# Kernel tuning notes

Measured on AMD Instinct MI355X. Metric: run time of the kernel, lower is better.

## Reference

```python
import jax, jax.numpy as jnp
import numpy as np

THRESHOLD = 0.5
NEG_POS_RATIO = 3
ALPHA = 1.0
B, P, C, O = 128, 8732, 21, 32


def xy_to_cxcy(xy):
    return jnp.concatenate([(xy[..., 2:] + xy[..., :2]) / 2, xy[..., 2:] - xy[..., :2]], axis=-1)


def cxcy_to_xy(cxcy):
    return jnp.concatenate([cxcy[..., :2] - cxcy[..., 2:] / 2, cxcy[..., :2] + cxcy[..., 2:] / 2], axis=-1)


def cxcy_to_gcxgcy(cxcy, priors_cxcy):
    g_cxcy = (cxcy[..., :2] - priors_cxcy[..., :2]) / (priors_cxcy[..., 2:] / 10.0)
    g_wh = jnp.log(cxcy[..., 2:] / priors_cxcy[..., 2:]) * 5.0
    return jnp.concatenate([g_cxcy, g_wh], axis=-1)


def find_jaccard_overlap(set1, set2):
    # set1: [O,4] xy, set2: [P,4] xy -> [O,P]
    lo = jnp.maximum(set1[:, None, :2], set2[None, :, :2])
    hi = jnp.minimum(set1[:, None, 2:], set2[None, :, 2:])
    inter = jnp.prod(jnp.clip(hi - lo, 0.0), axis=-1)
    a1 = jnp.prod(set1[:, 2:] - set1[:, :2], axis=-1)
    a2 = jnp.prod(set2[:, 2:] - set2[:, :2], axis=-1)
    union = a1[:, None] + a2[None, :] - inter
    return inter / union


def setup_inputs() -> dict:
    key = jax.random.key(0)
    k0, k1, k2, k3, k4, k5, k6 = jax.random.split(key, 7)
    predicted_locs = jax.random.normal(k0, (B, P, 4), jnp.float32)
    predicted_scores = jax.random.normal(k1, (B, P, C), jnp.float32)
    centers = jax.random.uniform(k2, (B, O, 2), jnp.float32, 0.2, 0.8)
    sizes = jax.random.uniform(k3, (B, O, 2), jnp.float32, 0.05, 0.3)
    boxes = jnp.concatenate([centers - sizes / 2, centers + sizes / 2], axis=-1)
    labels = jax.random.randint(k4, (B, O), 0, C)
    p_c = jax.random.uniform(k5, (P, 2), jnp.float32, 0.05, 0.95)
    p_wh = jax.random.uniform(k6, (P, 2), jnp.float32, 0.05, 0.5)
    priors_cxcy = jnp.concatenate([p_c, p_wh], axis=-1)
    return {"predicted_locs": predicted_locs, "predicted_scores": predicted_scores,
            "boxes": boxes, "labels": labels, "priors_cxcy": priors_cxcy}


def reference(predicted_locs, predicted_scores, boxes, labels, priors_cxcy):
    priors_xy = cxcy_to_xy(priors_cxcy)

    def match_one(boxes_i, labels_i):
        overlap = find_jaccard_overlap(boxes_i, priors_xy)           # [O,P]
        overlap_for_each_prior = jnp.max(overlap, axis=0)            # [P]
        object_for_each_prior = jnp.argmax(overlap, axis=0)          # [P]
        prior_for_each_object = jnp.argmax(overlap, axis=1)          # [O]
        object_for_each_prior = object_for_each_prior.at[prior_for_each_object].set(jnp.arange(O))
        overlap_for_each_prior = overlap_for_each_prior.at[prior_for_each_object].set(1.0)
        label_for_each_prior = labels_i[object_for_each_prior]
        label_for_each_prior = jnp.where(overlap_for_each_prior < THRESHOLD, 0, label_for_each_prior)
        true_locs_i = cxcy_to_gcxgcy(xy_to_cxcy(boxes_i[object_for_each_prior]), priors_cxcy)
        return label_for_each_prior, true_locs_i

    true_classes, true_locs = jax.vmap(match_one)(boxes, labels)     # [B,P], [B,P,4]

    positive = true_classes != 0                                     # [B,P]
    n_positives = jnp.sum(positive, axis=1)                          # [B]
    n_pos_total = jnp.sum(n_positives)

    # L1Loss (mean over selected positive elements, 4 per prior)
    abs_diff = jnp.abs(predicted_locs - true_locs)                   # [B,P,4]
    loc_loss = jnp.sum(abs_diff * positive[..., None]) / (n_pos_total.astype(jnp.float32) * 4.0)

    # per-element cross-entropy
    log_p = jax.nn.log_softmax(predicted_scores, axis=-1)            # [B,P,C]
    conf_loss_all = -jnp.take_along_axis(log_p, true_classes[..., None], axis=-1)[..., 0]  # [B,P]

    conf_loss_pos_sum = jnp.sum(jnp.where(positive, conf_loss_all, 0.0))
    conf_loss_neg = jnp.where(positive, 0.0, conf_loss_all)
    conf_loss_neg_sorted = -jnp.sort(-conf_loss_neg, axis=1)         # descending
    n_hard = NEG_POS_RATIO * n_positives                             # [B]
    hard_mask = jnp.arange(P)[None, :] < n_hard[:, None]             # [B,P]
    conf_loss_hard_neg_sum = jnp.sum(jnp.where(hard_mask, conf_loss_neg_sorted, 0.0))

    conf_loss = (conf_loss_hard_neg_sum + conf_loss_pos_sum) / n_pos_total.astype(jnp.float32)
    return conf_loss + ALPHA * loc_loss
```

## Files before the change

### kernel.cpp

```cpp
#include <hip/hip_runtime.h>
#include <hip/hip_bf16.h>

#define NB 128
#define NP 8732
#define NO 32
#define NC 21
#define NCHUNK 35


__device__ __forceinline__ float wave64_fmax_u(float m) {
    int v;
    v = __builtin_amdgcn_update_dpp(__float_as_int(m), __float_as_int(m), 0x111, 0xf, 0xf, false);
    m = fmaxf(m, __int_as_float(v));
    v = __builtin_amdgcn_update_dpp(__float_as_int(m), __float_as_int(m), 0x112, 0xf, 0xf, false);
    m = fmaxf(m, __int_as_float(v));
    v = __builtin_amdgcn_update_dpp(__float_as_int(m), __float_as_int(m), 0x114, 0xf, 0xf, false);
    m = fmaxf(m, __int_as_float(v));
    v = __builtin_amdgcn_update_dpp(__float_as_int(m), __float_as_int(m), 0x118, 0xf, 0xf, false);
    m = fmaxf(m, __int_as_float(v));
    v = __builtin_amdgcn_update_dpp(__float_as_int(m), __float_as_int(m), 0x142, 0xf, 0xf, false);
    m = fmaxf(m, __int_as_float(v));
    v = __builtin_amdgcn_update_dpp(__float_as_int(m), __float_as_int(m), 0x143, 0xf, 0xf, false);
    m = fmaxf(m, __int_as_float(v));
    return __int_as_float(__builtin_amdgcn_readlane(__float_as_int(m), 63));
}

__device__ __forceinline__ int wave64_imin_u(int m) {
    int v;
    v = __builtin_amdgcn_update_dpp(m, m, 0x111, 0xf, 0xf, false); m = v < m ? v : m;
    v = __builtin_amdgcn_update_dpp(m, m, 0x112, 0xf, 0xf, false); m = v < m ? v : m;
    v = __builtin_amdgcn_update_dpp(m, m, 0x114, 0xf, 0xf, false); m = v < m ? v : m;
    v = __builtin_amdgcn_update_dpp(m, m, 0x118, 0xf, 0xf, false); m = v < m ? v : m;
    v = __builtin_amdgcn_update_dpp(m, m, 0x142, 0xf, 0xf, false); m = v < m ? v : m;
    v = __builtin_amdgcn_update_dpp(m, m, 0x143, 0xf, 0xf, false); m = v < m ? v : m;
    return __builtin_amdgcn_readlane(m, 63);
}

__global__ __launch_bounds__(256) void k_code(const float* __restrict__ boxes,
                                              const float* __restrict__ priors,
                                              int* __restrict__ code) {
    int b = blockIdx.y;
    int tid = threadIdx.x;
    int base = blockIdx.x * 512 + tid;

    __shared__ float4 sbox[NO];
    if (tid < NO)
        sbox[tid] = ((const float4*)(boxes + (size_t)b * NO * 4))[tid];
    __syncthreads();

    float px1[2], py1[2], px2[2], py2[2], pa[2];
    float bestv[2];
    int   besto[2];
#pragma unroll
    for (int j = 0; j < 2; ++j) {
        int p = base + 256 * j;
        int pp = p < NP ? p : NP - 1;
        float4 pr = ((const float4*)priors)[pp];
        px1[j] = pr.x - pr.z * 0.5f; py1[j] = pr.y - pr.w * 0.5f;
        px2[j] = pr.x + pr.z * 0.5f; py2[j] = pr.y + pr.w * 0.5f;
        pa[j]  = (px2[j] - px1[j]) * (py2[j] - py1[j]);
        bestv[j] = -1.0f; besto[j] = 0;
    }

#pragma unroll
    for (int o = 0; o < NO; ++o) {
        float4 bx = sbox[o];
        float a1 = (bx.z - bx.x) * (bx.w - bx.y);
#pragma unroll
        for (int j = 0; j < 2; ++j) {
            float lx = fmaxf(bx.x, px1[j]), ly = fmaxf(bx.y, py1[j]);
            float hx = fminf(bx.z, px2[j]), hy = fminf(bx.w, py2[j]);
            float iw = fmaxf(hx - lx, 0.0f), ih = fmaxf(hy - ly, 0.0f);
            float inter = iw * ih;
            float iou = inter / (a1 + pa[j] - inter);
            if (iou > bestv[j]) { bestv[j] = iou; besto[j] = o; }
        }
    }
#pragma unroll
    for (int j = 0; j < 2; ++j) {
        int p = base + 256 * j;
        if (p < NP)
            code[(size_t)b * NP + p] = besto[j] | (bestv[j] >= 0.5f ? 256 : 0);
    }
}

__global__ __launch_bounds__(256) void k_obj(const float* __restrict__ boxes,
                                             const float* __restrict__ priors,
                                             int* __restrict__ pfor) {
    int b = blockIdx.y;
    int wid = threadIdx.x >> 6, lane = threadIdx.x & 63;
    int o = blockIdx.x * 4 + wid;

    float4 bx = ((const float4*)boxes)[b * NO + o];
    float a1 = (bx.z - bx.x) * (bx.w - bx.y);
    const float4* pr4 = (const float4*)priors;

    float bv = -1.0f; int bp = 0;
    for (int i = 0; i < 136; ++i) {
        int p = lane + (i << 6);
        float4 pr = pr4[p];
        float x1 = pr.x - pr.z * 0.5f, y1 = pr.y - pr.w * 0.5f;
        float x2 = pr.x + pr.z * 0.5f, y2 = pr.y + pr.w * 0.5f;
        float pa = (x2 - x1) * (y2 - y1);
        float lx = fmaxf(bx.x, x1), ly = fmaxf(bx.y, y1);
        float hx = fminf(bx.z, x2), hy = fminf(bx.w, y2);
        float inter = fmaxf(hx - lx, 0.0f) * fmaxf(hy - ly, 0.0f);
        float iou = inter / (a1 + pa - inter);
        if (iou > bv) { bv = iou; bp = p; }
    }
    {
        int p = lane + 8704;
        if (p < NP) {
            float4 pr = pr4[p];
            float x1 = pr.x - pr.z * 0.5f, y1 = pr.y - pr.w * 0.5f;
            float x2 = pr.x + pr.z * 0.5f, y2 = pr.y + pr.w * 0.5f;
            float pa = (x2 - x1) * (y2 - y1);
            float lx = fmaxf(bx.x, x1), ly = fmaxf(bx.y, y1);
            float hx = fminf(bx.z, x2), hy = fminf(bx.w, y2);
            float inter = fmaxf(hx - lx, 0.0f) * fmaxf(hy - ly, 0.0f);
            float iou = inter / (a1 + pa - inter);
            if (iou > bv) { bv = iou; bp = p; }
        }
    }
    float m = wave64_fmax_u(bv);
    int pc = (bv == m) ? bp : 0x7FFFFFFF;
    int mp = wave64_imin_u(pc);
    if (lane == 0) pfor[b * NO + o] = mp;
}

__global__ __launch_bounds__(256) void k_loss(const float* __restrict__ plocs,
                                              const float* __restrict__ scores,
                                              const float* __restrict__ boxes,
                                              const int* __restrict__ labels,
                                              const float* __restrict__ priors,
                                              const int* __restrict__ code,
                                              const int* __restrict__ pfor,
                                              float* __restrict__ confneg,
                                              int* __restrict__ pnp,
                                              double* __restrict__ pd0,
                                              double* __restrict__ pd1,
                                              int* __restrict__ donecnt) {
    __shared__ float srow[256 * NC];
    __shared__ int spfl[NO];
    int b = blockIdx.y;
    int p0 = blockIdx.x * 256;
    int cnt = NP - p0; if (cnt > 256) cnt = 256;
    int nf4 = cnt * NC / 4;
    const float4* src4 = (const float4*)(scores + ((size_t)b * NP + p0) * NC);
    for (int i = threadIdx.x; i < nf4; i += 256)
        ((float4*)srow)[i] = src4[i];
    if (threadIdx.x < NO)
        spfl[threadIdx.x] = pfor[b * NO + threadIdx.x];
    __syncthreads();

    int p = p0 + threadIdx.x;
    float posconf = 0.0f, locpart = 0.0f;
    int isp = 0;

    if (p < NP) {
        int cd = code[(size_t)b * NP + p];
        int obj = cd & 255;
        int mat = cd >> 8;
#pragma unroll
        for (int o = 0; o < NO; ++o)
            if (spfl[o] == p) { obj = o; mat = 1; }
        int lbl = mat ? labels[b * NO + obj] : 0;

        const float* s = srow + threadIdx.x * NC;
        float m = s[0];
#pragma unroll
        for (int c = 1; c < NC; ++c) m = fmaxf(m, s[c]);
        float sum = 0.0f;
#pragma unroll
        for (int c = 0; c < NC; ++c) sum += __expf(s[c] - m);
        float conf = m + __logf(sum) - s[lbl];

        if (lbl != 0) {
            isp = 1;
            posconf = conf;
            float4 bx = ((const float4*)boxes)[b * NO + obj];
            float4 pr = ((const float4*)priors)[p];
            float cx = (bx.x + bx.z) * 0.5f, cy = (bx.y + bx.w) * 0.5f;
            float w = bx.z - bx.x, h = bx.w - bx.y;
            float gx = (cx - pr.x) / (pr.z * 0.1f);
            float gy = (cy - pr.y) / (pr.w * 0.1f);
            float gw = __logf(w / pr.z) * 5.0f;
            float gh = __logf(h / pr.w) * 5.0f;
            float4 pl = ((const float4*)plocs)[(size_t)b * NP + p];
            locpart = fabsf(pl.x - gx) + fabsf(pl.y - gy) +
                      fabsf(pl.z - gw) + fabsf(pl.w - gh);
        }
        confneg[(size_t)b * NP + p] = isp ? 0.0f : conf;
    }

    for (int s = 32; s > 0; s >>= 1) {
        posconf += __shfl_xor(posconf, s, 64);
        locpart += __shfl_xor(locpart, s, 64);
        isp     += __shfl_xor(isp, s, 64);
    }
    __shared__ float w0[4], w1[4];
    __shared__ int wc[4];
    int wid = threadIdx.x >> 6, lane = threadIdx.x & 63;
    if (lane == 0) { w0[wid] = posconf; w1[wid] = locpart; wc[wid] = isp; }
    __syncthreads();
    if (threadIdx.x == 0) {
        int pb = b * NCHUNK + blockIdx.x;
        pd0[pb] = (double)(w0[0] + w0[1] + w0[2] + w0[3]);
        pd1[pb] = (double)(w1[0] + w1[1] + w1[2] + w1[3]);
        pnp[pb] = wc[0] + wc[1] + wc[2] + wc[3];
        if (pb == 0) *donecnt = 0;
    }
}

__global__ __launch_bounds__(256) void k_topk(const float* __restrict__ confneg,
                                              const int* __restrict__ pnp,
                                              const double* __restrict__ pd0,
                                              const double* __restrict__ pd1,
                                              int* __restrict__ snp,
                                              double* __restrict__ sums,
                                              int* __restrict__ donecnt,
                                              float* __restrict__ out) {
    __shared__ int    si2[2][4];
    __shared__ int    siw[4];
    __shared__ double sdd[4];
    __shared__ int    sk;
    int tid = threadIdx.x, b = blockIdx.x;
    int lane = tid & 63, wid = tid >> 6;

    if (wid == 0) {
        int np_ = 0; double d0 = 0.0, d1 = 0.0;
        if (lane < NCHUNK) {
            int pb = b * NCHUNK + lane;
            np_ = pnp[pb]; d0 = pd0[pb]; d1 = pd1[pb];
        }
        for (int s = 32; s > 0; s >>= 1) {
            np_ += __shfl_xor(np_, s, 64);
            d0  += __shfl_xor(d0, s, 64);
            d1  += __shfl_xor(d1, s, 64);
        }
        if (lane == 0) {
            int k = np_ * 3; if (k > NP) k = NP;
            sk = k;
            snp[b] = np_;
            sums[b * 3 + 1] = d0;
            sums[b * 3 + 2] = d1;
        }
    }

    const float* src = confneg + (size_t)b * NP;
    float val[35];
#pragma unroll
    for (int j = 0; j < 35; ++j) {
        int i = tid + j * 256;
        val[j] = (i < NP) ? src[i] : 0.0f;
    }
    __syncthreads();
    int k = sk;

    double hn = 0.0;
    if (k > 0) {
        unsigned T = 0;
        int par = 0;
        for (int bit = 30; bit >= 0; --bit) {
            unsigned cand = T | (1u << bit);
            int cnt = 0;
#pragma unroll
            for (int j = 0; j < 35; ++j)
                cnt += __popcll(__ballot(__float_as_uint(val[j]) >= cand));
            if (lane == 0) si2[par][wid] = cnt;
            __syncthreads();
            int t = si2[par][0] + si2[par][1] + si2[par][2] + si2[par][3];
            par ^= 1;
            if (t >= k) T = cand;
        }

        int cgt = 0;
        double sgt = 0.0;
#pragma unroll
        for (int j = 0; j < 35; ++j) {
            unsigned u = __float_as_uint(val[j]);
            if (u > T) { cgt++; sgt += (double)val[j]; }
        }
        for (int s = 32; s > 0; s >>= 1) {
            cgt += __shfl_xor(cgt, s, 64);
            sgt += __shfl_xor(sgt, s, 64);
        }
        if (lane == 0) { siw[wid] = cgt; sdd[wid] = sgt; }
        __syncthreads();
        if (tid == 0) {
            int cg = siw[0] + siw[1] + siw[2] + siw[3];
            double sg = sdd[0] + sdd[1] + sdd[2] + sdd[3];
            hn = sg + (double)(k - cg) * (double)__uint_as_float(T);
        }
    }
    if (tid == 0) sums[b * 3 + 0] = hn;

    __shared__ int samlast;
    if (tid == 0) {
        __threadfence();
        int prev = atomicAdd(donecnt, 1);
        samlast = (prev == NB - 1) ? 1 : 0;
    }
    __syncthreads();
    if (!samlast) return;
    __threadfence();

    double hnn = 0.0, pc = 0.0, lc = 0.0, npd = 0.0;
    if (tid < NB) {
        hnn = atomicAdd(&sums[tid * 3 + 0], 0.0);
        pc  = atomicAdd(&sums[tid * 3 + 1], 0.0);
        lc  = atomicAdd(&sums[tid * 3 + 2], 0.0);
        npd = (double)atomicAdd((int*)&snp[tid], 0);
    }
    for (int s = 32; s > 0; s >>= 1) {
        hnn += __shfl_xor(hnn, s, 64);
        pc  += __shfl_xor(pc, s, 64);
        lc  += __shfl_xor(lc, s, 64);
        npd += __shfl_xor(npd, s, 64);
    }
    __shared__ double sfin[4][2];
    if (lane == 0 && wid < 2) {
        sfin[0][wid] = hnn; sfin[1][wid] = pc; sfin[2][wid] = lc; sfin[3][wid] = npd;
    }
    __syncthreads();
    if (tid == 0) {
        double H  = sfin[0][0] + sfin[0][1];
        double P  = sfin[1][0] + sfin[1][1];
        double L  = sfin[2][0] + sfin[2][1];
        double nt = sfin[3][0] + sfin[3][1];
        out[0] = (float)((H + P) / nt + L / (nt * 4.0));
    }
}

extern "C" void kernel_launch(void* const* d_in, const int* in_sizes, int n_in,
                              void* d_out, int out_size, void* d_ws, size_t ws_size,
                              hipStream_t stream) {
    const float* plocs  = (const float*)d_in[0];
    const float* scores = (const float*)d_in[1];
    const float* boxes  = (const float*)d_in[2];
    const int*   labels = (const int*)d_in[3];
    const float* priors = (const float*)d_in[4];
    float* out = (float*)d_out;

    char* ws = (char*)d_ws;
    int*    pfor    = (int*)ws;
    double* pd0     = (double*)(ws + 16384);
    double* pd1     = (double*)(ws + 52224);
    int*    pnp     = (int*)(ws + 88064);
    int*    snp     = (int*)(ws + 105984);
    double* sums    = (double*)(ws + 106496);
    int*    donecnt = (int*)(ws + 109568);
    int*    code    = (int*)(ws + 109824);
    float*  confneg = (float*)(ws + 4580608);

    hipLaunchKernelGGL(k_code, dim3((NP + 511) / 512, NB), dim3(256), 0, stream,
                       boxes, priors, code);
    hipLaunchKernelGGL(k_obj, dim3(NO / 4, NB), dim3(256), 0, stream,
                       boxes, priors, pfor);
    hipLaunchKernelGGL(k_loss, dim3(NCHUNK, NB), dim3(256), 0, stream,
                       plocs, scores, boxes, labels, priors, code, pfor,
                       confneg, pnp, pd0, pd1, donecnt);
    hipLaunchKernelGGL(k_topk, dim3(NB), dim3(256), 0, stream,
                       confneg, pnp, pd0, pd1, snp, sums, donecnt, out);
}
```

Before: 240.1 us.

## Fuse prior matching into loss kernel, tile k_obj over LDS, widen topk blocks

```diff
diff --git a/kernel.cpp b/kernel.cpp
--- a/kernel.cpp
+++ b/kernel.cpp
@@ -36,96 +36,59 @@
     return __builtin_amdgcn_readlane(m, 63);
 }
 
-__global__ __launch_bounds__(256) void k_code(const float* __restrict__ boxes,
-                                              const float* __restrict__ priors,
-                                              int* __restrict__ code) {
-    int b = blockIdx.y;
-    int tid = threadIdx.x;
-    int base = blockIdx.x * 512 + tid;
-
-    __shared__ float4 sbox[NO];
-    if (tid < NO)
-        sbox[tid] = ((const float4*)(boxes + (size_t)b * NO * 4))[tid];
-    __syncthreads();
-
-    float px1[2], py1[2], px2[2], py2[2], pa[2];
-    float bestv[2];
-    int   besto[2];
-#pragma unroll
-    for (int j = 0; j < 2; ++j) {
-        int p = base + 256 * j;
-        int pp = p < NP ? p : NP - 1;
-        float4 pr = ((const float4*)priors)[pp];
-        px1[j] = pr.x - pr.z * 0.5f; py1[j] = pr.y - pr.w * 0.5f;
-        px2[j] = pr.x + pr.z * 0.5f; py2[j] = pr.y + pr.w * 0.5f;
-        pa[j]  = (px2[j] - px1[j]) * (py2[j] - py1[j]);
-        bestv[j] = -1.0f; besto[j] = 0;
-    }
-
-#pragma unroll
-    for (int o = 0; o < NO; ++o) {
-        float4 bx = sbox[o];
-        float a1 = (bx.z - bx.x) * (bx.w - bx.y);
-#pragma unroll
-        for (int j = 0; j < 2; ++j) {
-            float lx = fmaxf(bx.x, px1[j]), ly = fmaxf(bx.y, py1[j]);
-            float hx = fminf(bx.z, px2[j]), hy = fminf(bx.w, py2[j]);
-            float iw = fmaxf(hx - lx, 0.0f), ih = fmaxf(hy - ly, 0.0f);
-            float inter = iw * ih;
-            float iou = inter / (a1 + pa[j] - inter);
-            if (iou > bestv[j]) { bestv[j] = iou; besto[j] = o; }
-        }
-    }
-#pragma unroll
-    for (int j = 0; j < 2; ++j) {
-        int p = base + 256 * j;
-        if (p < NP)
-            code[(size_t)b * NP + p] = besto[j] | (bestv[j] >= 0.5f ? 256 : 0);
-    }
-}
-
 __global__ __launch_bounds__(256) void k_obj(const float* __restrict__ boxes,
                                              const float* __restrict__ priors,
                                              int* __restrict__ pfor) {
+    __shared__ float4 spr[1024];
     int b = blockIdx.y;
-    int wid = threadIdx.x >> 6, lane = threadIdx.x & 63;
-    int o = blockIdx.x * 4 + wid;
-
-    float4 bx = ((const float4*)boxes)[b * NO + o];
-    float a1 = (bx.z - bx.x) * (bx.w - bx.y);
-    const float4* pr4 = (const float4*)priors;
-
-    float bv = -1.0f; int bp = 0;
-    for (int i = 0; i < 136; ++i) {
-        int p = lane + (i << 6);
-        float4 pr = pr4[p];
-        float x1 = pr.x - pr.z * 0.5f, y1 = pr.y - pr.w * 0.5f;
-        float x2 = pr.x + pr.z * 0.5f, y2 = pr.y + pr.w * 0.5f;
-        float pa = (x2 - x1) * (y2 - y1);
-        float lx = fmaxf(bx.x, x1), ly = fmaxf(bx.y, y1);
-        float hx = fminf(bx.z, x2), hy = fminf(bx.w, y2);
-        float inter = fmaxf(hx - lx, 0.0f) * fmaxf(hy - ly, 0.0f);
-        float iou = inter / (a1 + pa - inter);
-        if (iou > bv) { bv = iou; bp = p; }
-    }
-    {
-        int p = lane + 8704;
-        if (p < NP) {
-            float4 pr = pr4[p];
+    int tid = threadIdx.x, lane = tid & 63, wid = tid >> 6;
+    int o0 = blockIdx.x * 8 + wid * 2;
+
+    float4 bx0 = ((const float4*)boxes)[b * NO + o0];
+    float4 bx1 = ((const float4*)boxes)[b * NO + o0 + 1];
+    float a10 = (bx0.z - bx0.x) * (bx0.w - bx0.y);
+    float a11 = (bx1.z - bx1.x) * (bx1.w - bx1.y);
+
+    float bv0 = -1.0f, bv1 = -1.0f;
+    int   bp0 = 0,     bp1 = 0;
+
+    for (int c0 = 0; c0 < NP; c0 += 1024) {
+        int n = NP - c0; if (n > 1024) n = 1024;
+        __syncthreads();
+        for (int i = tid; i < n; i += 256)
+            spr[i] = ((const float4*)priors)[c0 + i];
+        __syncthreads();
+#pragma unroll 4
+        for (int i = lane; i < n; i += 64) {
+            float4 pr = spr[i];
             float x1 = pr.x - pr.z * 0.5f, y1 = pr.y - pr.w * 0.5f;
             float x2 = pr.x + pr.z * 0.5f, y2 = pr.y + pr.w * 0.5f;
             float pa = (x2 - x1) * (y2 - y1);
-            float lx = fmaxf(bx.x, x1), ly = fmaxf(bx.y, y1);
-            float hx = fminf(bx.z, x2), hy = fminf(bx.w, y2);
-            float inter = fmaxf(hx - lx, 0.0f) * fmaxf(hy - ly, 0.0f);
-            float iou = inter / (a1 + pa - inter);
-            if (iou > bv) { bv = iou; bp = p; }
-        }
-    }
-    float m = wave64_fmax_u(bv);
-    int pc = (bv == m) ? bp : 0x7FFFFFFF;
-    int mp = wave64_imin_u(pc);
-    if (lane == 0) pfor[b * NO + o] = mp;
+            int p = c0 + i;
+            {
+                float lx = fmaxf(bx0.x, x1), ly = fmaxf(bx0.y, y1);
+                float hx = fminf(bx0.z, x2), hy = fminf(bx0.w, y2);
+                float inter = fmaxf(hx - lx, 0.0f) * fmaxf(hy - ly, 0.0f);
+                float iou = inter / (a10 + pa - inter);
+                if (iou > bv0) { bv0 = iou; bp0 = p; }
+            }
+            {
+                float lx = fmaxf(bx1.x, x1), ly = fmaxf(bx1.y, y1);
+                float hx = fminf(bx1.z, x2), hy = fminf(bx1.w, y2);
+                float inter = fmaxf(hx - lx, 0.0f) * fmaxf(hy - ly, 0.0f);
+                float iou = inter / (a11 + pa - inter);
+                if (iou > bv1) { bv1 = iou; bp1 = p; }
+            }
+        }
+    }
+    float m0 = wave64_fmax_u(bv0);
+    int mp0 = wave64_imin_u((bv0 == m0) ? bp0 : 0x7FFFFFFF);
+    float m1 = wave64_fmax_u(bv1);
+    int mp1 = wave64_imin_u((bv1 == m1) ? bp1 : 0x7FFFFFFF);
+    if (lane == 0) {
+        pfor[b * NO + o0]     = mp0;
+        pfor[b * NO + o0 + 1] = mp1;
+    }
 }
 
 __global__ __launch_bounds__(256) void k_loss(const float* __restrict__ plocs,
@@ -133,7 +96,6 @@
                                               const float* __restrict__ boxes,
                                               const int* __restrict__ labels,
                                               const float* __restrict__ priors,
-                                              const int* __restrict__ code,
                                               const int* __restrict__ pfor,
                                               float* __restrict__ confneg,
                                               int* __restrict__ pnp,
@@ -141,6 +103,7 @@
                                               double* __restrict__ pd1,
                                               int* __restrict__ donecnt) {
     __shared__ float srow[256 * NC];
+    __shared__ float4 sbox[NO];
     __shared__ int spfl[NO];
     int b = blockIdx.y;
     int p0 = blockIdx.x * 256;
@@ -149,8 +112,10 @@
     const float4* src4 = (const float4*)(scores + ((size_t)b * NP + p0) * NC);
     for (int i = threadIdx.x; i < nf4; i += 256)
         ((float4*)srow)[i] = src4[i];
-    if (threadIdx.x < NO)
+    if (threadIdx.x < NO) {
+        sbox[threadIdx.x] = ((const float4*)boxes)[b * NO + threadIdx.x];
         spfl[threadIdx.x] = pfor[b * NO + threadIdx.x];
+    }
     __syncthreads();
 
     int p = p0 + threadIdx.x;
@@ -158,9 +123,24 @@
     int isp = 0;
 
     if (p < NP) {
-        int cd = code[(size_t)b * NP + p];
-        int obj = cd & 255;
-        int mat = cd >> 8;
+        float4 pr = ((const float4*)priors)[p];
+        float px1 = pr.x - pr.z * 0.5f, py1 = pr.y - pr.w * 0.5f;
+        float px2 = pr.x + pr.z * 0.5f, py2 = pr.y + pr.w * 0.5f;
+        float pa  = (px2 - px1) * (py2 - py1);
+
+        float bestv = -1.0f; int besto = 0;
+#pragma unroll
+        for (int o = 0; o < NO; ++o) {
+            float4 bx = sbox[o];
+            float a1 = (bx.z - bx.x) * (bx.w - bx.y);
+            float lx = fmaxf(bx.x, px1), ly = fmaxf(bx.y, py1);
+            float hx = fminf(bx.z, px2), hy = fminf(bx.w, py2);
+            float inter = fmaxf(hx - lx, 0.0f) * fmaxf(hy - ly, 0.0f);
+            float iou = inter / (a1 + pa - inter);
+            if (iou > bestv) { bestv = iou; besto = o; }
+        }
+        int obj = besto;
+        int mat = bestv >= 0.5f ? 1 : 0;
 #pragma unroll
         for (int o = 0; o < NO; ++o)
             if (spfl[o] == p) { obj = o; mat = 1; }
@@ -178,8 +158,7 @@
         if (lbl != 0) {
             isp = 1;
             posconf = conf;
-            float4 bx = ((const float4*)boxes)[b * NO + obj];
-            float4 pr = ((const float4*)priors)[p];
+            float4 bx = sbox[obj];
             float cx = (bx.x + bx.z) * 0.5f, cy = (bx.y + bx.w) * 0.5f;
             float w = bx.z - bx.x, h = bx.w - bx.y;
             float gx = (cx - pr.x) / (pr.z * 0.1f);
@@ -212,17 +191,17 @@
     }
 }
 
-__global__ __launch_bounds__(256) void k_topk(const float* __restrict__ confneg,
-                                              const int* __restrict__ pnp,
-                                              const double* __restrict__ pd0,
-                                              const double* __restrict__ pd1,
-                                              int* __restrict__ snp,
-                                              double* __restrict__ sums,
-                                              int* __restrict__ donecnt,
-                                              float* __restrict__ out) {
-    __shared__ int    si2[2][4];
-    __shared__ int    siw[4];
-    __shared__ double sdd[4];
+__global__ __launch_bounds__(1024) void k_topk(const float* __restrict__ confneg,
+                                               const int* __restrict__ pnp,
+                                               const double* __restrict__ pd0,
+                                               const double* __restrict__ pd1,
+                                               int* __restrict__ snp,
+                                               double* __restrict__ sums,
+                                               int* __restrict__ donecnt,
+                                               float* __restrict__ out) {
+    __shared__ int    si2[2][16];
+    __shared__ int    siw[16];
+    __shared__ double sdd[16];
     __shared__ int    sk;
     int tid = threadIdx.x, b = blockIdx.x;
     int lane = tid & 63, wid = tid >> 6;
@@ -248,10 +227,10 @@
     }
 
     const float* src = confneg + (size_t)b * NP;
-    float val[35];
-#pragma unroll
-    for (int j = 0; j < 35; ++j) {
-        int i = tid + j * 256;
+    float val[9];
+#pragma unroll
+    for (int j = 0; j < 9; ++j) {
+        int i = tid + j * 1024;
         val[j] = (i < NP) ? src[i] : 0.0f;
     }
     __syncthreads();
@@ -265,11 +244,13 @@
             unsigned cand = T | (1u << bit);
             int cnt = 0;
 #pragma unroll
-            for (int j = 0; j < 35; ++j)
+            for (int j = 0; j < 9; ++j)
                 cnt += __popcll(__ballot(__float_as_uint(val[j]) >= cand));
             if (lane == 0) si2[par][wid] = cnt;
             __syncthreads();
-            int t = si2[par][0] + si2[par][1] + si2[par][2] + si2[par][3];
+            int t = 0;
+#pragma unroll
+            for (int w = 0; w < 16; ++w) t += si2[par][w];
             par ^= 1;
             if (t >= k) T = cand;
         }
@@ -277,7 +258,7 @@
         int cgt = 0;
         double sgt = 0.0;
 #pragma unroll
-        for (int j = 0; j < 35; ++j) {
+        for (int j = 0; j < 9; ++j) {
             unsigned u = __float_as_uint(val[j]);
             if (u > T) { cgt++; sgt += (double)val[j]; }
         }
@@ -288,8 +269,8 @@
         if (lane == 0) { siw[wid] = cgt; sdd[wid] = sgt; }
         __syncthreads();
         if (tid == 0) {
-            int cg = siw[0] + siw[1] + siw[2] + siw[3];
-            double sg = sdd[0] + sdd[1] + sdd[2] + sdd[3];
+            int cg = 0; double sg = 0.0;
+            for (int w = 0; w < 16; ++w) { cg += siw[w]; sg += sdd[w]; }
             hn = sg + (double)(k - cg) * (double)__uint_as_float(T);
         }
     }
@@ -350,16 +331,13 @@
     int*    snp     = (int*)(ws + 105984);
     double* sums    = (double*)(ws + 106496);
     int*    donecnt = (int*)(ws + 109568);
-    int*    code    = (int*)(ws + 109824);
-    float*  confneg = (float*)(ws + 4580608);
-
-    hipLaunchKernelGGL(k_code, dim3((NP + 511) / 512, NB), dim3(256), 0, stream,
-                       boxes, priors, code);
-    hipLaunchKernelGGL(k_obj, dim3(NO / 4, NB), dim3(256), 0, stream,
+    float*  confneg = (float*)(ws + 109824);
+
+    hipLaunchKernelGGL(k_obj, dim3(NO / 8, NB), dim3(256), 0, stream,
                        boxes, priors, pfor);
     hipLaunchKernelGGL(k_loss, dim3(NCHUNK, NB), dim3(256), 0, stream,
-                       plocs, scores, boxes, labels, priors, code, pfor,
+                       plocs, scores, boxes, labels, priors, pfor,
                        confneg, pnp, pd0, pd1, donecnt);
-    hipLaunchKernelGGL(k_topk, dim3(NB), dim3(256), 0, stream,
+    hipLaunchKernelGGL(k_topk, dim3(NB), dim3(1024), 0, stream,
                        confneg, pnp, pd0, pd1, snp, sums, donecnt, out);
 }
```

Result: faster. 227.6 us (-5.2%).
